# Optimization experiments

Measured on AMD Instinct MI355X. Metric: run time of the kernel, lower is better.

## Reference

```python
import jax, jax.numpy as jnp
import numpy as np

N = 50000
D = 128
E = 600000

def setup_inputs() -> dict:
    key = jax.random.key(0)
    k1, k2, k3, k4, k5 = jax.random.split(key, 5)
    z1 = jax.random.normal(k1, (N, D), dtype=jnp.float32)
    z2 = jax.random.normal(k2, (N, D), dtype=jnp.float32)
    adj_row = jax.random.randint(k3, (E,), 0, N, dtype=jnp.int32)
    adj_col = jax.random.randint(k4, (E,), 0, N, dtype=jnp.int32)
    adj_val = jax.random.uniform(k5, (E,), dtype=jnp.float32)
    a = jnp.full((N, D), 0.5, dtype=jnp.float32)
    b = jnp.full((N, D), 0.5, dtype=jnp.float32)
    alpha = jnp.float32(0.5)
    return {"z1": z1, "z2": z2, "adj_row": adj_row, "adj_col": adj_col,
            "adj_val": adj_val, "a": a, "b": b, "alpha": alpha}

def reference(z1, z2, adj_row, adj_col, adj_val, a, b, alpha):
    # elementwise gated combine: z_i = a*z1 + b*z2   [N, D]
    z_i = a * z1 + b * z2
    # sparse matmul: z_l[r] = sum_e adj_val[e] * z_i[adj_col[e]] for adj_row[e]==r
    msgs = adj_val[:, None] * z_i[adj_col]          # [E, D]
    z_l = jax.ops.segment_sum(msgs, adj_row, num_segments=N)  # [N, D]
    # residual blend
    return alpha * z_l + (1.0 - alpha) * z_i
```

## Files before the change

kernel.cpp:

```cpp
#include <hip/hip_runtime.h>
#include <hip/hip_fp16.h>

#define DDIM 128
#define CAPMAX 32

__global__ void __launch_bounds__(256) build_kernel(
    const float4* __restrict__ z1, const float4* __restrict__ z2,
    const float4* __restrict__ a,  const float4* __restrict__ b,
    float4* __restrict__ zi32, uint2* __restrict__ zi16, int n4,
    const int* __restrict__ rows, const int* __restrict__ cols,
    const float* __restrict__ vals,
    int2* __restrict__ slots, int* __restrict__ cnt,
    int* __restrict__ ohead, int* __restrict__ onext,
    int cap, int E) {
  const int t = (blockIdx.x >> 1) * blockDim.x + threadIdx.x;
  const int stride = (gridDim.x >> 1) * blockDim.x;
  if (blockIdx.x & 1) {
    for (int e = t; e < E; e += stride) {
      const int r = rows[e];
      const int j = atomicAdd(&cnt[r], 1);
      if (j < cap) {
        int2 s;
        s.x = cols[e];
        s.y = __float_as_int(vals[e]);
        slots[(size_t)r * cap + j] = s;
      } else {
        onext[e] = atomicExch(&ohead[r], e + 1);
      }
    }
  } else {
    for (int j = t; j < n4; j += stride) {
      float4 A = a[j], B = b[j], X = z1[j], Y = z2[j];
      float4 z;
      z.x = A.x * X.x + B.x * Y.x;
      z.y = A.y * X.y + B.y * Y.y;
      z.z = A.z * X.z + B.z * Y.z;
      z.w = A.w * X.w + B.w * Y.w;
      zi32[j] = z;
      __half2 h0 = __floats2half2_rn(z.x, z.y);
      __half2 h1 = __floats2half2_rn(z.z, z.w);
      uint2 pk;
      pk.x = *reinterpret_cast<unsigned*>(&h0);
      pk.y = *reinterpret_cast<unsigned*>(&h1);
      zi16[j] = pk;
    }
  }
}

__global__ void __launch_bounds__(256) reduce_kernel(
    const int2* __restrict__ slots, const int* __restrict__ cnt,
    const int* __restrict__ ohead, const int* __restrict__ onext,
    const int* __restrict__ cols, const float* __restrict__ vals,
    const float* __restrict__ alpha_p,
    const __half2* __restrict__ zi16, const float2* __restrict__ zi32,
    float2* __restrict__ out2, int cap, int N) {
  const int r = (int)((blockIdx.x * blockDim.x + threadIdx.x) >> 6);
  const int lane = threadIdx.x & 63;
  if (r >= N) return;
  const float alpha = alpha_p[0];

  const int deg = cnt[r];
  const int m = deg < cap ? deg : cap;
  const int2* sp = slots + (size_t)r * cap;
  const int4* sp4 = (const int4*)sp;

  float2 a0 = make_float2(0.f, 0.f), a1 = a0, a2 = a0, a3 = a0;
  float2 a4 = a0, a5 = a0, a6 = a0, a7 = a0;
  int j = 0;
  for (; j + 8 <= m; j += 8) {
    const int4 p0 = sp4[(j >> 1) + 0];
    const int4 p1 = sp4[(j >> 1) + 1];
    const int4 p2 = sp4[(j >> 1) + 2];
    const int4 p3 = sp4[(j >> 1) + 3];
    const __half2 g0 = zi16[(size_t)p0.x * (DDIM / 2) + lane];
    const __half2 g1 = zi16[(size_t)p0.z * (DDIM / 2) + lane];
    const __half2 g2 = zi16[(size_t)p1.x * (DDIM / 2) + lane];
    const __half2 g3 = zi16[(size_t)p1.z * (DDIM / 2) + lane];
    const __half2 g4 = zi16[(size_t)p2.x * (DDIM / 2) + lane];
    const __half2 g5 = zi16[(size_t)p2.z * (DDIM / 2) + lane];
    const __half2 g6 = zi16[(size_t)p3.x * (DDIM / 2) + lane];
    const __half2 g7 = zi16[(size_t)p3.z * (DDIM / 2) + lane];
    const float2 f0 = __half22float2(g0), f1 = __half22float2(g1);
    const float2 f2 = __half22float2(g2), f3 = __half22float2(g3);
    const float2 f4 = __half22float2(g4), f5 = __half22float2(g5);
    const float2 f6 = __half22float2(g6), f7 = __half22float2(g7);
    const float v0 = __int_as_float(p0.y), v1 = __int_as_float(p0.w);
    const float v2 = __int_as_float(p1.y), v3 = __int_as_float(p1.w);
    const float v4 = __int_as_float(p2.y), v5 = __int_as_float(p2.w);
    const float v6 = __int_as_float(p3.y), v7 = __int_as_float(p3.w);
    a0.x += v0 * f0.x; a0.y += v0 * f0.y;
    a1.x += v1 * f1.x; a1.y += v1 * f1.y;
    a2.x += v2 * f2.x; a2.y += v2 * f2.y;
    a3.x += v3 * f3.x; a3.y += v3 * f3.y;
    a4.x += v4 * f4.x; a4.y += v4 * f4.y;
    a5.x += v5 * f5.x; a5.y += v5 * f5.y;
    a6.x += v6 * f6.x; a6.y += v6 * f6.y;
    a7.x += v7 * f7.x; a7.y += v7 * f7.y;
  }
  for (; j < m; ++j) {
    const int2 s = sp[j];
    const float v = __int_as_float(s.y);
    const float2 f = __half22float2(zi16[(size_t)s.x * (DDIM / 2) + lane]);
    a0.x += v * f.x; a0.y += v * f.y;
  }
  if (deg > cap) {
    int e1 = ohead[r];
    while (e1 > 0) {
      const int e = e1 - 1;
      e1 = onext[e];
      const int c = cols[e];
      const float v = vals[e];
      const float2 f = __half22float2(zi16[(size_t)c * (DDIM / 2) + lane]);
      a0.x += v * f.x; a0.y += v * f.y;
    }
  }

  float2 acc;
  acc.x = ((a0.x + a1.x) + (a2.x + a3.x)) + ((a4.x + a5.x) + (a6.x + a7.x));
  acc.y = ((a0.y + a1.y) + (a2.y + a3.y)) + ((a4.y + a5.y) + (a6.y + a7.y));
  const float2 zr = zi32[(size_t)r * (DDIM / 2) + lane];
  const float om = 1.0f - alpha;
  float2 o;
  o.x = alpha * acc.x + om * zr.x;
  o.y = alpha * acc.y + om * zr.y;
  out2[(size_t)r * (DDIM / 2) + lane] = o;
}

extern "C" void kernel_launch(void* const* d_in, const int* in_sizes, int n_in,
                              void* d_out, int out_size, void* d_ws, size_t ws_size,
                              hipStream_t stream) {
  const float* z1    = (const float*)d_in[0];
  const float* z2    = (const float*)d_in[1];
  const int*   rows  = (const int*)  d_in[2];
  const int*   cols  = (const int*)  d_in[3];
  const float* vals  = (const float*)d_in[4];
  const float* a     = (const float*)d_in[5];
  const float* b     = (const float*)d_in[6];
  const float* alpha = (const float*)d_in[7];
  float* out = (float*)d_out;

  const int ND = in_sizes[0];
  const int E  = in_sizes[2];
  const int N  = ND / DDIM;
  const int n4 = ND / 4;

  float* zi32 = (float*)d_ws;
  __half2* zi16 = (__half2*)(zi32 + ND);
  int* cnt   = (int*)((char*)zi16 + (size_t)ND * 2);
  int* ohead = cnt + N;
  int* onext = ohead + N;
  int2* slots = (int2*)(onext + E);

  const size_t fixed_bytes = (size_t)ND * 4 + (size_t)ND * 2 +
                             ((size_t)2 * N + E) * 4;
  size_t avail = ws_size > fixed_bytes ? ws_size - fixed_bytes : 0;
  int cap = (int)(avail / ((size_t)N * sizeof(int2)));
  if (cap > CAPMAX) cap = CAPMAX;
  cap &= ~1;
  if (cap < 2) cap = 0;

  hipMemsetAsync(cnt, 0x00, (size_t)2 * N * sizeof(int), stream);

  build_kernel<<<2048, 256, 0, stream>>>(
      (const float4*)z1, (const float4*)z2, (const float4*)a,
      (const float4*)b, (float4*)zi32, (uint2*)zi16, n4,
      rows, cols, vals, slots, cnt, ohead, onext, cap, E);

  const int blocks2 = (int)(((long long)N * 64 + 255) / 256);
  reduce_kernel<<<blocks2, 256, 0, stream>>>(
      slots, cnt, ohead, onext, cols, vals, alpha,
      zi16, (const float2*)zi32, (float2*)out, cap, N);
}
```

Baseline: 199.6 us.

## Drop fp32 zi buffer and recompute residual from inputs in reduce kernel

Removes the fp32 copy of z_i written by the build kernel. The reduce kernel now recomputes the residual term from z1, z2, a and b directly. Build blocks are rebalanced to three dense blocks per edge block, and the dense loop is unrolled by two. This trades one 25 MB write and read for reading four input arrays in the reduce kernel, which increases total traffic there.

```diff
diff --git a/kernel.cpp b/kernel.cpp
--- a/kernel.cpp
+++ b/kernel.cpp
@@ -7,15 +7,15 @@
 __global__ void __launch_bounds__(256) build_kernel(
     const float4* __restrict__ z1, const float4* __restrict__ z2,
     const float4* __restrict__ a,  const float4* __restrict__ b,
-    float4* __restrict__ zi32, uint2* __restrict__ zi16, int n4,
+    uint2* __restrict__ zi16, int n4,
     const int* __restrict__ rows, const int* __restrict__ cols,
     const float* __restrict__ vals,
     int2* __restrict__ slots, int* __restrict__ cnt,
     int* __restrict__ ohead, int* __restrict__ onext,
     int cap, int E) {
-  const int t = (blockIdx.x >> 1) * blockDim.x + threadIdx.x;
-  const int stride = (gridDim.x >> 1) * blockDim.x;
-  if (blockIdx.x & 1) {
+  if ((blockIdx.x & 3) == 3) {
+    const int t = (int)(blockIdx.x >> 2) * blockDim.x + threadIdx.x;
+    const int stride = (int)(gridDim.x >> 2) * blockDim.x;
     for (int e = t; e < E; e += stride) {
       const int r = rows[e];
       const int j = atomicAdd(&cnt[r], 1);
@@ -29,16 +29,36 @@
       }
     }
   } else {
-    for (int j = t; j < n4; j += stride) {
+    const int dense = (int)blockIdx.x - (int)(blockIdx.x >> 2);
+    const int t = dense * blockDim.x + threadIdx.x;
+    const int stride = (int)((gridDim.x >> 2) * 3) * blockDim.x;
+    int j = t;
+    for (; j + stride < n4; j += 2 * stride) {
+      const int k = j + stride;
+      float4 A0 = a[j], B0 = b[j], X0 = z1[j], Y0 = z2[j];
+      float4 A1 = a[k], B1 = b[k], X1 = z1[k], Y1 = z2[k];
+      __half2 h00 = __floats2half2_rn(A0.x * X0.x + B0.x * Y0.x,
+                                      A0.y * X0.y + B0.y * Y0.y);
+      __half2 h01 = __floats2half2_rn(A0.z * X0.z + B0.z * Y0.z,
+                                      A0.w * X0.w + B0.w * Y0.w);
+      __half2 h10 = __floats2half2_rn(A1.x * X1.x + B1.x * Y1.x,
+                                      A1.y * X1.y + B1.y * Y1.y);
+      __half2 h11 = __floats2half2_rn(A1.z * X1.z + B1.z * Y1.z,
+                                      A1.w * X1.w + B1.w * Y1.w);
+      uint2 p0, p1;
+      p0.x = *reinterpret_cast<unsigned*>(&h00);
+      p0.y = *reinterpret_cast<unsigned*>(&h01);
+      p1.x = *reinterpret_cast<unsigned*>(&h10);
+      p1.y = *reinterpret_cast<unsigned*>(&h11);
+      zi16[j] = p0;
+      zi16[k] = p1;
+    }
+    for (; j < n4; j += stride) {
       float4 A = a[j], B = b[j], X = z1[j], Y = z2[j];
-      float4 z;
-      z.x = A.x * X.x + B.x * Y.x;
-      z.y = A.y * X.y + B.y * Y.y;
-      z.z = A.z * X.z + B.z * Y.z;
-      z.w = A.w * X.w + B.w * Y.w;
-      zi32[j] = z;
-      __half2 h0 = __floats2half2_rn(z.x, z.y);
-      __half2 h1 = __floats2half2_rn(z.z, z.w);
+      __half2 h0 = __floats2half2_rn(A.x * X.x + B.x * Y.x,
+                                     A.y * X.y + B.y * Y.y);
+      __half2 h1 = __floats2half2_rn(A.z * X.z + B.z * Y.z,
+                                     A.w * X.w + B.w * Y.w);
       uint2 pk;
       pk.x = *reinterpret_cast<unsigned*>(&h0);
       pk.y = *reinterpret_cast<unsigned*>(&h1);
@@ -52,12 +72,20 @@
     const int* __restrict__ ohead, const int* __restrict__ onext,
     const int* __restrict__ cols, const float* __restrict__ vals,
     const float* __restrict__ alpha_p,
-    const __half2* __restrict__ zi16, const float2* __restrict__ zi32,
+    const __half2* __restrict__ zi16,
+    const float2* __restrict__ z1_2, const float2* __restrict__ z2_2,
+    const float2* __restrict__ a_2,  const float2* __restrict__ b_2,
     float2* __restrict__ out2, int cap, int N) {
   const int r = (int)((blockIdx.x * blockDim.x + threadIdx.x) >> 6);
   const int lane = threadIdx.x & 63;
   if (r >= N) return;
   const float alpha = alpha_p[0];
+
+  const size_t rb = (size_t)r * (DDIM / 2) + lane;
+  const float2 rz1 = z1_2[rb];
+  const float2 rz2 = z2_2[rb];
+  const float2 raa = a_2[rb];
+  const float2 rbb = b_2[rb];
 
   const int deg = cnt[r];
   const int m = deg < cap ? deg : cap;
@@ -118,11 +146,10 @@
   float2 acc;
   acc.x = ((a0.x + a1.x) + (a2.x + a3.x)) + ((a4.x + a5.x) + (a6.x + a7.x));
   acc.y = ((a0.y + a1.y) + (a2.y + a3.y)) + ((a4.y + a5.y) + (a6.y + a7.y));
-  const float2 zr = zi32[(size_t)r * (DDIM / 2) + lane];
   const float om = 1.0f - alpha;
   float2 o;
-  o.x = alpha * acc.x + om * zr.x;
-  o.y = alpha * acc.y + om * zr.y;
+  o.x = alpha * acc.x + om * (raa.x * rz1.x + rbb.x * rz2.x);
+  o.y = alpha * acc.y + om * (raa.y * rz1.y + rbb.y * rz2.y);
   out2[(size_t)r * (DDIM / 2) + lane] = o;
 }
 
@@ -144,15 +171,13 @@
   const int N  = ND / DDIM;
   const int n4 = ND / 4;
 
-  float* zi32 = (float*)d_ws;
-  __half2* zi16 = (__half2*)(zi32 + ND);
-  int* cnt   = (int*)((char*)zi16 + (size_t)ND * 2);
+  __half2* zi16 = (__half2*)d_ws;
+  int* cnt   = (int*)((char*)d_ws + (size_t)ND * 2);
   int* ohead = cnt + N;
   int* onext = ohead + N;
   int2* slots = (int2*)(onext + E);
 
-  const size_t fixed_bytes = (size_t)ND * 4 + (size_t)ND * 2 +
-                             ((size_t)2 * N + E) * 4;
+  const size_t fixed_bytes = (size_t)ND * 2 + ((size_t)2 * N + E) * 4;
   size_t avail = ws_size > fixed_bytes ? ws_size - fixed_bytes : 0;
   int cap = (int)(avail / ((size_t)N * sizeof(int2)));
   if (cap > CAPMAX) cap = CAPMAX;
@@ -163,11 +188,13 @@
 
   build_kernel<<<2048, 256, 0, stream>>>(
       (const float4*)z1, (const float4*)z2, (const float4*)a,
-      (const float4*)b, (float4*)zi32, (uint2*)zi16, n4,
+      (const float4*)b, (uint2*)zi16, n4,
       rows, cols, vals, slots, cnt, ohead, onext, cap, E);
 
   const int blocks2 = (int)(((long long)N * 64 + 255) / 256);
   reduce_kernel<<<blocks2, 256, 0, stream>>>(
-      slots, cnt, ohead, onext, cols, vals, alpha,
-      zi16, (const float2*)zi32, (float2*)out, cap, N);
+      slots, cnt, ohead, onext, cols, vals, alpha, zi16,
+      (const float2*)z1, (const float2*)z2,
+      (const float2*)a,  (const float2*)b,
+      (float2*)out, cap, N);
 }
```

Result: slower. 239.8 us (+20.2%).
